# Kernel tuning notes

Measured on AMD Instinct MI355X. Metric: run time of the kernel, lower is better.

The kernel has to match this reference:

```python
import jax, jax.numpy as jnp
import numpy as np

DN = ('NCHW', 'OIHW', 'NCHW')


def conv(x, W, s, p):
    return jax.lax.conv_general_dilated(x, W, (s, s), [(p, p), (p, p)], dimension_numbers=DN)


def conv_t(y, W, s, p, op):
    # F.conv_transpose2d(y, W, stride=s, padding=p, output_padding=op)
    k = W.shape[2]
    Wt = jnp.flip(W, (2, 3)).transpose(1, 0, 2, 3)  # (I,O,k,k) -> OIHW for the transpose conv
    pad = (k - 1 - p, k - 1 - p + op)
    return jax.lax.conv_general_dilated(y, Wt, (1, 1), [pad, pad], lhs_dilation=(s, s), dimension_numbers=DN)


def build_blk(weight_specs, ms, g, n):
    # blk_diag[r, c, g, m, n'] accumulation exactly as in the torch nested loops
    blk = jnp.zeros((ms, ms, g, n, n), dtype=weight_specs[0][0].dtype)
    for (W, stride, k) in weight_specs:
        A = W.reshape(W.shape[0], g, n, k, k)  # (O, g, n, k, k)
        ATA = jnp.einsum('ogmab,ognab->abgmn', A, A)  # (k, k, g, n, n)
        offset = ((stride - k) // 2) % stride  # k odd branch of the torch code
        for i1 in range(k):
            for j1 in range(k):
                for r in range((i1 + offset) % stride, ms, stride):
                    for c in range((j1 + offset) % stride, ms, stride):
                        blk = blk.at[r, c].add(ATA[i1, j1])
    return blk


def sub_diag(Z, X, blk, ms, g, n):
    b, c, h, w = X.shape
    X0 = X.reshape(b, g, n, h // ms, ms, w // ms, ms)
    Yd = jnp.einsum('rcgmn,bgnhrwc->bgmhrwc', blk, X0)
    return Z - Yd.reshape(b, c, h, w)


def hollow_forward(x0, x1, W00, W10, W11, b0, b1, g):
    # multiply: Y_i = sum_j conv(X_j)
    Y0 = conv(x0, W00, 1, 2)                       # (B,16,258,258)
    Y1 = conv(x0, W10, 2, 3) + conv(x1, W11, 1, 2)  # (B,32,130,130)
    # multiply_transpose: Z_j = sum_i conv_t(Y_i)
    Z0 = conv_t(Y0, W00, 1, 2, 0) + conv_t(Y1, W10, 2, 3, 1)  # (B,16,256,256)
    Z1 = conv_t(Y1, W11, 1, 2, 0)                             # (B,32,128,128)
    # block-diagonal self-term subtraction
    blk0 = build_blk([(W00, 1, 3), (W10, 2, 3)], ms=2, g=1, n=16)
    blk1 = build_blk([(W11, 1, 3)], ms=1, g=2, n=16)
    Z0 = sub_diag(Z0, x0, blk0, 2, 1, 16)
    Z1 = sub_diag(Z1, x1, blk1, 1, 2, 16)
    # bias term: y -= bias/||bias|| * g[i]; return -y
    Z0 = Z0 - (b0 / jnp.linalg.norm(b0)) * g[0]
    Z1 = Z1 - (b1 / jnp.linalg.norm(b1)) * g[1]
    return (-Z0, -Z1)


def setup_inputs() -> dict:
    key = jax.random.key(0)
    ks = jax.random.split(key, 8)
    B = 16
    x0 = jax.random.normal(ks[0], (B, 16, 256, 256), dtype=jnp.float32)
    x1 = jax.random.normal(ks[1], (B, 32, 128, 128), dtype=jnp.float32)
    # conv weights (PyTorch OIHW layout), modest scale ~ 1/sqrt(fan_in*k*k)
    W00 = jax.random.normal(ks[2], (16, 16, 3, 3), dtype=jnp.float32) * 0.08
    W10 = jax.random.normal(ks[3], (32, 16, 3, 3), dtype=jnp.float32) * 0.08
    W11 = jax.random.normal(ks[4], (32, 32, 3, 3), dtype=jnp.float32) * 0.06
    b0 = jax.random.uniform(ks[5], (16, 256, 256), dtype=jnp.float32)
    b1 = jax.random.uniform(ks[6], (32, 128, 128), dtype=jnp.float32)
    g = jnp.ones((2,), dtype=jnp.float32)
    return {'x0': x0, 'x1': x1, 'W00': W00, 'W10': W10, 'W11': W11, 'b0': b0, 'b1': b1, 'g': g}


def reference(x0, x1, W00, W10, W11, b0, b1, g):
    return hollow_forward(x0, x1, W00, W10, W11, b0, b1, g)
```

## Files before the change

kernel.cpp:

```cpp
#include <hip/hip_runtime.h>
#include <stdint.h>


using short8 = __attribute__((ext_vector_type(8))) short;
using f32x4  = __attribute__((ext_vector_type(4))) float;

#define B_ 16

static constexpr size_t Y1T_OFF  = 0;
static constexpr size_t Y1T_ROWB = 132 * 64;
static constexpr size_t X1T_OFF  = (size_t)16 * 130 * 132 * 64;
static constexpr size_t AB0_OFF  = X1T_OFF + (size_t)16 * 128 * 128 * 64;
static constexpr size_t AB1_OFF  = AB0_OFF + 24 * 1024;
static constexpr size_t SUM_OFF  = AB1_OFF + 20 * 1024;
static constexpr size_t AB2_OFF  = SUM_OFF + 1024;

__device__ __forceinline__ uint32_t bf16rne(float v) {
  uint32_t u = __float_as_uint(v);
  return (u + 0x7fffu + ((u >> 16) & 1u)) >> 16;
}
__device__ __forceinline__ uint32_t packbf(float lo, float hi) {
  return bf16rne(lo) | (bf16rne(hi) << 16);
}
__device__ __forceinline__ f32x4 mfma16(short8 a, short8 b, f32x4 c) {
  return __builtin_amdgcn_mfma_f32_16x16x32_bf16(a, b, c, 0, 0, 0);
}
__device__ __forceinline__ int xcd_swz(int bid, int chunk) {
  return (bid & 7) * chunk + (bid >> 3);
}

__global__ void blob_k(const float* __restrict__ W00, const float* __restrict__ W10,
                       const float* __restrict__ W11, char* __restrict__ ws) {
  int e = blockIdx.x * 256 + threadIdx.x;
  if (e < 2) ((float*)(ws + SUM_OFF))[e] = 0.f;
  if (e < 12288) {
    int chunk = e >> 9, le = e & 511, lane = le >> 3, j = le & 7;
    int q = lane >> 4, m = lane & 15;
    float val = 0.f;
    if (chunk < 13) {
      int t = 2 * chunk + (q >> 1);
      int n = ((q & 1) << 3) + j;
      if (t <= 24 && t != 12) {
        int dy = t / 5 - 2, dx = t % 5 - 2;
        for (int o = 0; o < 16; ++o) {
          const float* wm = W00 + (o * 16 + m) * 9;
          const float* wn = W00 + (o * 16 + n) * 9;
          for (int ay = 0; ay < 3; ++ay) {
            int ay2 = ay + dy; if ((unsigned)ay2 > 2u) continue;
            for (int ax = 0; ax < 3; ++ax) {
              int ax2 = ax + dx; if ((unsigned)ax2 > 2u) continue;
              val += wm[ay * 3 + ax] * wn[ay2 * 3 + ax2];
            }
          }
        }
      }
    } else if (chunk < 22) {
      int tap = chunk - 13;
      int o = ((lane >> 4) << 3) + j;
      val = W10[(o * 16 + m) * 9 + tap];
    } else {
      int py = chunk - 22;
      int k = ((lane >> 4) << 3) + j;
      int par = k >> 4, n = k & 15;
      for (int o = 0; o < 32; ++o) {
        const float* wn = W10 + (o * 16 + n) * 9;
        const float* wm = W10 + (o * 16 + m) * 9;
        for (int by = 0; by < 3; ++by) {
          if ((py == 0) ? (by != 1) : (by == 1)) continue;
          for (int bx = 0; bx < 3; ++bx) {
            if ((par == 0) ? (bx != 1) : (bx == 1)) continue;
            val -= wn[by * 3 + bx] * wm[by * 3 + bx];
          }
        }
      }
    }
    ((uint16_t*)(ws + AB0_OFF))[chunk * 512 + lane * 8 + j] = (uint16_t)bf16rne(val);
  } else if (e < 12288 + 10240) {
    int e2 = e - 12288;
    int chunk = e2 >> 10, r = e2 & 1023, h = r >> 9, le = r & 511;
    int lane = le >> 3, j = le & 7;
    int m = h * 16 + (lane & 15);
    int kk = ((lane >> 4) << 3) + j;
    float val = 0.f;
    if (chunk < 9) {
      val = W11[(kk * 32 + m) * 9 + chunk];
    } else if ((kk >> 4) == h) {
      int np = kk & 15;
      float s = 0.f;
      for (int o = 0; o < 32; ++o)
        for (int t = 0; t < 9; ++t)
          s += W11[(o * 32 + m) * 9 + t] * W11[(o * 32 + h * 16 + np) * 9 + t];
      val = -s;
    }
    ((uint16_t*)(ws + AB1_OFF))[(chunk * 2 + h) * 512 + lane * 8 + j] = (uint16_t)bf16rne(val);
  } else if (e < 12288 + 10240 + 28672) {
    int e3 = e - 22528;
    int chunk = e3 >> 9, le = e3 & 511;
    int lane = le >> 3, j = le & 7;
    int q = lane >> 4, m = lane & 15;
    int k = q * 8 + j;
    int part;
    float val = 0.f;
    if (chunk < 36) {
      int t = chunk >> 2, h = (chunk >> 1) & 1;
      part = chunk & 1;
      int o = h * 16 + m;
      val = W11[(o * 32 + k) * 9 + t];
    } else {
      int c2 = chunk - 36;
      int c5 = c2 >> 2, h = (c2 >> 1) & 1;
      part = c2 & 1;
      int tap = 2 * c5 + (k >> 4);
      int o = h * 16 + m;
      if (tap <= 8) val = W10[(o * 16 + (k & 15)) * 9 + tap];
    }
    uint32_t hi = bf16rne(val);
    uint16_t outv;
    if (part == 0) outv = (uint16_t)hi;
    else outv = (uint16_t)bf16rne(val - __uint_as_float(hi << 16));
    ((uint16_t*)(ws + AB2_OFF))[chunk * 512 + lane * 8 + j] = outv;
  }
}

__global__ void sumsq_k(const float* __restrict__ src, int n, float* __restrict__ dst) {
  float s = 0.f;
  for (int i = blockIdx.x * blockDim.x + threadIdx.x; i < n; i += gridDim.x * blockDim.x) {
    float v = src[i];
    s += v * v;
  }
  #pragma unroll
  for (int off = 32; off > 0; off >>= 1) s += __shfl_down(s, off, 64);
  if ((threadIdx.x & 63) == 0) atomicAdd(dst, s);
}

__global__ __launch_bounds__(256) void x1t_k(const float* __restrict__ x1, char* __restrict__ ws) {
  __shared__ __align__(16) uint16_t tmp[128 * 32];
  int b = blockIdx.x >> 7, r = blockIdx.x & 127;
  int tid = threadIdx.x;
  for (int e = tid; e < 4096; e += 256) {
    int ch = e >> 7, c = e & 127;
    float v = x1[((size_t)(b * 32 + ch) * 128 + r) * 128 + c];
    tmp[c * 32 + ch] = (uint16_t)bf16rne(v);
  }
  __syncthreads();
  char* dst = ws + X1T_OFF + ((size_t)(b * 128 + r) * 128) * 64;
  for (int e = tid; e < 512; e += 256)
    *(short8*)(dst + e * 16) = *(const short8*)((const char*)tmp + e * 16);
}

__global__ __launch_bounds__(256, 5) void y1m_k(const float* __restrict__ x0,
                                                char* __restrict__ ws) {
  __shared__ __align__(16) uint16_t x0s[2 * 3 * 2 * 146 * 8];
  int tid = threadIdx.x;
  int bid = xcd_swz(blockIdx.x, 260);
  int b = bid / 130, iy = bid % 130;

  {
    uint4 z = make_uint4(0u, 0u, 0u, 0u);
    for (int e = tid; e < 1752; e += 256) ((uint4*)x0s)[e] = z;
  }
  __syncthreads();

  {
    const float* x0b = x0 + (size_t)b * 1048576;
    for (int e = tid; e < 6144; e += 256) {
      int r = e >> 11;
      int ch0 = ((e >> 8) & 7) * 2;
      int c = e & 255;
      int gy = 2 * iy + r - 3;
      float v0 = 0.f, v1 = 0.f;
      if ((unsigned)gy < 256u) {
        const float* rp = x0b + (size_t)ch0 * 65536 + (size_t)gy * 256 + c;
        v0 = rp[0]; v1 = rp[65536];
      }
      int sc = c + 3, p = sc & 1, hc = sc >> 1;
      *(uint32_t*)((char*)x0s + ((((ch0 >> 3) * 3 + r) * 2 + p) * 146 + hc) * 16 + (ch0 & 7) * 2)
          = packbf(v0, v1);
    }
  }

  int lane = tid & 63, wv = tid >> 6;
  int nn = lane & 15, q = lane >> 4, qh = q >> 1, ql = q & 1;
  const char* ab2 = ws + AB2_OFF;
  const char* x1tb = ws + X1T_OFF;

  f32x4 a00 = {0.f,0.f,0.f,0.f}, a01 = {0.f,0.f,0.f,0.f};
  f32x4 a10 = {0.f,0.f,0.f,0.f}, a11 = {0.f,0.f,0.f,0.f};
  f32x4 a20 = {0.f,0.f,0.f,0.f}, a21 = {0.f,0.f,0.f,0.f};
  const short8 z8 = {0,0,0,0,0,0,0,0};

  #pragma unroll
  for (int t = 0; t < 9; ++t) {
    const int ay = t / 3, ax = t % 3;
    const char* cb = ab2 + t * 4096 + lane * 16;
    short8 Ah0 = *(const short8*)(cb);
    short8 Al0 = *(const short8*)(cb + 1024);
    short8 Ah1 = *(const short8*)(cb + 2048);
    short8 Al1 = *(const short8*)(cb + 3072);
    int gy = iy + ay - 2;
    bool rowok = ((unsigned)gy < 128u);
    const char* rb = x1tb + ((size_t)(b * 128 + (rowok ? gy : 0))) * 8192 + q * 16;
    int c0 = (wv << 4) + nn + ax - 2;
    bool ok0 = rowok && ((unsigned)c0 < 128u);
    short8 B0 = *(const short8*)(rb + (size_t)(ok0 ? c0 : 0) * 64);
    if (!ok0) B0 = z8;
    int c1 = c0 + 64;
    bool ok1 = rowok && ((unsigned)c1 < 128u);
    short8 B1 = *(const short8*)(rb + (size_t)(ok1 ? c1 : 0) * 64);
    if (!ok1) B1 = z8;
    a00 = mfma16(Ah0, B0, a00); a00 = mfma16(Al0, B0, a00);
    a01 = mfma16(Ah1, B0, a01); a01 = mfma16(Al1, B0, a01);
    a10 = mfma16(Ah0, B1, a10); a10 = mfma16(Al0, B1, a10);
    a11 = mfma16(Ah1, B1, a11); a11 = mfma16(Al1, B1, a11);
    if (wv == 0) {
      int c2 = c0 + 128;
      bool ok2 = rowok && ((unsigned)c2 < 128u);
      short8 B2 = *(const short8*)(rb + (size_t)(ok2 ? c2 : 0) * 64);
      if (!ok2) B2 = z8;
      a20 = mfma16(Ah0, B2, a20); a20 = mfma16(Al0, B2, a20);
      a21 = mfma16(Ah1, B2, a21); a21 = mfma16(Al1, B2, a21);
    }
  }

  __syncthreads();

  #pragma unroll
  for (int c5 = 0; c5 < 5; ++c5) {
    const char* cb = ab2 + (36 + c5 * 4) * 1024 + lane * 16;
    short8 Ah0 = *(const short8*)(cb);
    short8 Al0 = *(const short8*)(cb + 1024);
    short8 Ah1 = *(const short8*)(cb + 2048);
    short8 Al1 = *(const short8*)(cb + 3072);
    int tl = 2 * c5 + qh; if (tl > 8) tl = 8;
    int by = tl / 3, bx = tl % 3;
    int p = bx & 1, hb = bx >> 1;
    const char* bb = (const char*)x0s + ((((ql * 3 + by) * 2 + p) * 146) + hb + nn) * 16 + wv * 256;
    short8 B0 = *(const short8*)(bb);
    short8 B1 = *(const short8*)(bb + 1024);
    a00 = mfma16(Ah0, B0, a00); a00 = mfma16(Al0, B0, a00);
    a01 = mfma16(Ah1, B0, a01); a01 = mfma16(Al1, B0, a01);
    a10 = mfma16(Ah0, B1, a10); a10 = mfma16(Al0, B1, a10);
    a11 = mfma16(Ah1, B1, a11); a11 = mfma16(Al1, B1, a11);
    if (wv == 0) {
      short8 B2 = *(const short8*)(bb + 2048);
      a20 = mfma16(Ah0, B2, a20); a20 = mfma16(Al0, B2, a20);
      a21 = mfma16(Ah1, B2, a21); a21 = mfma16(Al1, B2, a21);
    }
  }

  char* yp = ws + Y1T_OFF + (size_t)(b * 130 + iy) * Y1T_ROWB;
  auto st = [&](int f, f32x4 v0, f32x4 v1) {
    int ix = f * 16 + nn;
    if (ix < 130) {
      uint64_t lo = (uint64_t)packbf(v0[0], v0[1]) | ((uint64_t)packbf(v0[2], v0[3]) << 32);
      uint64_t hi = (uint64_t)packbf(v1[0], v1[1]) | ((uint64_t)packbf(v1[2], v1[3]) << 32);
      *(uint64_t*)(yp + ix * 64 + q * 8) = lo;
      *(uint64_t*)(yp + ix * 64 + 32 + q * 8) = hi;
    }
  };
  st(wv, a00, a01);
  st(wv + 4, a10, a11);
  if (wv == 0) st(8, a20, a21);
}

__global__ __launch_bounds__(256, 5) void out0_k(const float* __restrict__ x0,
                                                 const float* __restrict__ b0,
                                                 const float* __restrict__ gg,
                                                 const char* __restrict__ ws,
                                                 float* __restrict__ out) {
  __shared__ __align__(16) uint16_t x0s[2 * 5 * 132 * 8];
  __shared__ __align__(16) uint16_t y1s[4 * 2 * 66 * 8];
  int tid = threadIdx.x;
  int bid = xcd_swz(blockIdx.x, 1024);
  int b = bid >> 9, jy = (bid >> 1) & 255;
  int jx_base = (bid & 1) << 7;

  {
    const float* x0b = x0 + (size_t)b * 1048576;
    for (int e = tid; e < 1320; e += 256) {
      int c = e % 132, rr = e / 132, r = rr % 5, oct = rr / 5;
      int gy = jy + r - 2, gx = jx_base + c - 2;
      uint32_t w0 = 0u, w1 = 0u, w2 = 0u, w3 = 0u;
      if ((unsigned)gy < 256u && (unsigned)gx < 256u) {
        const float* p = x0b + (size_t)(oct * 8) * 65536 + gy * 256 + gx;
        w0 = packbf(p[0],      p[65536]);
        w1 = packbf(p[131072], p[196608]);
        w2 = packbf(p[262144], p[327680]);
        w3 = packbf(p[393216], p[458752]);
      }
      *(uint4*)((char*)x0s + (size_t)e * 16) = make_uint4(w0, w1, w2, w3);
    }
  }
  {
    const char* y1tb = ws + Y1T_OFF;
    int uy = jy >> 1, c0 = jx_base >> 1;
    for (int e = tid; e < 528; e += 256) {
      int qq = e & 3, t = e >> 2, lc = t % 66, ry = t / 66;
      short8 v = *(const short8*)(y1tb +
          ((size_t)(b * 130 + uy + 1 + ry) * 132 + c0 + lc) * 64 + qq * 16);
      *(short8*)((char*)y1s + ((size_t)(qq * 2 + ry) * 66 + lc) * 16) = v;
    }
  }
  __syncthreads();

  int lane = tid & 63, wv = tid >> 6;
  int nn = lane & 15, q = lane >> 4, qh = q >> 1, ql = q & 1;
  const char* ab0 = ws + AB0_OFF;
  f32x4 acc[2];
  #pragma unroll
  for (int i = 0; i < 2; ++i) { acc[i][0]=0.f; acc[i][1]=0.f; acc[i][2]=0.f; acc[i][3]=0.f; }

  const uint16_t* xsl = x0s + ql * 5280;
  const uint16_t* ysl = y1s + q * 1056;
  int pxb = wv * 32 + nn;

  #pragma unroll
  for (int c = 0; c < 13; ++c) {
    short8 A = *(const short8*)(ab0 + c * 1024 + lane * 16);
    const int tA = 2 * c;
    const int tB = (2 * c + 1 > 24) ? 24 : 2 * c + 1;
    const int offA = ((tA / 5) * 132 + (tA % 5)) * 8;
    const int offB = ((tB / 5) * 132 + (tB % 5)) * 8;
    int toff = qh ? offB : offA;
    const uint16_t* base = xsl + toff + pxb * 8;
    short8 B0 = *(const short8*)(base);
    short8 B1 = *(const short8*)(base + 128);
    acc[0] = mfma16(A, B0, acc[0]);
    acc[1] = mfma16(A, B1, acc[1]);
  }

  {
    const short8 z8 = {0,0,0,0,0,0,0,0};
    if ((jy & 1) == 0) {
      #pragma unroll
      for (int bx = 0; bx < 3; ++bx) {
        short8 A = *(const short8*)(ab0 + (16 + bx) * 1024 + lane * 16);
        bool keep = (((nn + 3 - bx) & 1) == 0);
        int cb = (nn + 3 - bx) >> 1;
        const uint16_t* base = ysl + (cb + wv * 16) * 8;
        short8 B0 = *(const short8*)(base);
        short8 B1 = *(const short8*)(base + 64);
        if (!keep) { B0 = z8; B1 = z8; }
        acc[0] = mfma16(A, B0, acc[0]);
        acc[1] = mfma16(A, B1, acc[1]);
      }
    } else {
      #pragma unroll
      for (int s = 0; s < 2; ++s) {
        const int chunkb = s ? 19 : 13;
        const int rybase = s ? 0 : 1;
        #pragma unroll
        for (int bx = 0; bx < 3; ++bx) {
          short8 A = *(const short8*)(ab0 + (chunkb + bx) * 1024 + lane * 16);
          bool keep = (((nn + 3 - bx) & 1) == 0);
          int cb = (nn + 3 - bx) >> 1;
          const uint16_t* base = ysl + (rybase * 66 + cb + wv * 16) * 8;
          short8 B0 = *(const short8*)(base);
          short8 B1 = *(const short8*)(base + 64);
          if (!keep) { B0 = z8; B1 = z8; }
          acc[0] = mfma16(A, B0, acc[0]);
          acc[1] = mfma16(A, B1, acc[1]);
        }
      }
    }
  }

  {
    const short8 z8 = {0,0,0,0,0,0,0,0};
    short8 A = *(const short8*)(ab0 + (22 + (jy & 1)) * 1024 + lane * 16);
    const uint16_t* base = xsl + (2 * 132 + 2) * 8 + pxb * 8;
    short8 B0 = *(const short8*)(base);
    short8 B1 = *(const short8*)(base + 128);
    bool keep = ((nn & 1) == qh);
    if (!keep) { B0 = z8; B1 = z8; }
    acc[0] = mfma16(A, B0, acc[0]);
    acc[1] = mfma16(A, B1, acc[1]);
  }

  float rs0 = gg[0] / sqrtf(((const float*)(ws + SUM_OFF))[0]);
  #pragma unroll
  for (int i = 0; i < 2; ++i) {
    int px = jx_base + wv * 32 + i * 16 + nn;
    #pragma unroll
    for (int reg = 0; reg < 4; ++reg) {
      int m = q * 4 + reg;
      size_t boff = ((size_t)m * 256 + jy) * 256 + px;
      out[((size_t)(b * 16 + m) * 256 + jy) * 256 + px] = b0[boff] * rs0 - acc[i][reg];
    }
  }
}

__global__ __launch_bounds__(256) void out1_k(const float* __restrict__ b1,
                                              const float* __restrict__ gg,
                                              const char* __restrict__ ws,
                                              float* __restrict__ out) {
  __shared__ __align__(16) uint16_t ys[4 * 3 * 132 * 8];
  __shared__ __align__(16) uint16_t x1s[4 * 128 * 8];
  int tid = threadIdx.x;
  int bid = xcd_swz(blockIdx.x, 256);
  int b = bid >> 7, jy = bid & 127;
  const char* y1tb = ws + Y1T_OFF;
  const char* x1tb = ws + X1T_OFF;
  for (int e = tid; e < 1584; e += 256) {
    int row = e / 528, rr = e % 528, c = rr >> 2, qq = rr & 3;
    short8 v = *(const short8*)(y1tb + ((size_t)(b * 130 + jy + row) * 132 + c) * 64 + qq * 16);
    *(short8*)(ys + qq * 3168 + (row * 132 + c) * 8) = v;
  }
  for (int e = tid; e < 512; e += 256) {
    int c = e >> 2, qq = e & 3;
    short8 v = *(const short8*)(x1tb + ((size_t)(b * 128 + jy) * 128 + c) * 64 + qq * 16);
    *(short8*)(x1s + qq * 1024 + c * 8) = v;
  }
  __syncthreads();

  int lane = tid & 63, wv = tid >> 6;
  int nn = lane & 15, q = lane >> 4;
  const char* ab1 = ws + AB1_OFF;
  f32x4 acc[2][2];
  #pragma unroll
  for (int i = 0; i < 2; ++i)
    #pragma unroll
    for (int h = 0; h < 2; ++h) { acc[i][h][0]=0.f; acc[i][h][1]=0.f; acc[i][h][2]=0.f; acc[i][h][3]=0.f; }

  const uint16_t* ysl = ys + q * 3168;
  const uint16_t* xsl = x1s + q * 1024;
  int pxb = wv * 32 + nn;

  #pragma unroll
  for (int t = 0; t < 9; ++t) {
    const int ay = t / 3, ax = t % 3;
    short8 A0 = *(const short8*)(ab1 + (t * 2 + 0) * 1024 + lane * 16);
    short8 A1 = *(const short8*)(ab1 + (t * 2 + 1) * 1024 + lane * 16);
    const uint16_t* base = ysl + ((2 - ay) * 132 + (2 - ax) + pxb) * 8;
    short8 B0 = *(const short8*)(base);
    short8 B1 = *(const short8*)(base + 128);
    acc[0][0] = mfma16(A0, B0, acc[0][0]);
    acc[0][1] = mfma16(A1, B0, acc[0][1]);
    acc[1][0] = mfma16(A0, B1, acc[1][0]);
    acc[1][1] = mfma16(A1, B1, acc[1][1]);
  }
  {
    short8 A0 = *(const short8*)(ab1 + 18 * 1024 + lane * 16);
    short8 A1 = *(const short8*)(ab1 + 19 * 1024 + lane * 16);
    const uint16_t* base = xsl + pxb * 8;
    short8 B0 = *(const short8*)(base);
    short8 B1 = *(const short8*)(base + 128);
    acc[0][0] = mfma16(A0, B0, acc[0][0]);
    acc[0][1] = mfma16(A1, B0, acc[0][1]);
    acc[1][0] = mfma16(A0, B1, acc[1][0]);
    acc[1][1] = mfma16(A1, B1, acc[1][1]);
  }

  float rs1 = gg[1] / sqrtf(((const float*)(ws + SUM_OFF))[1]);
  #pragma unroll
  for (int i = 0; i < 2; ++i) {
    int px = wv * 32 + i * 16 + nn;
    #pragma unroll
    for (int h = 0; h < 2; ++h)
      #pragma unroll
      for (int reg = 0; reg < 4; ++reg) {
        int m = h * 16 + q * 4 + reg;
        size_t boff = ((size_t)m * 128 + jy) * 128 + px;
        out[16777216 + ((size_t)(b * 32 + m) * 128 + jy) * 128 + px] = b1[boff] * rs1 - acc[i][h][reg];
      }
  }
}

extern "C" void kernel_launch(void* const* d_in, const int* in_sizes, int n_in,
                              void* d_out, int out_size, void* d_ws, size_t ws_size,
                              hipStream_t stream) {
  const float* x0  = (const float*)d_in[0];
  const float* x1  = (const float*)d_in[1];
  const float* W00 = (const float*)d_in[2];
  const float* W10 = (const float*)d_in[3];
  const float* W11 = (const float*)d_in[4];
  const float* b0  = (const float*)d_in[5];
  const float* b1  = (const float*)d_in[6];
  const float* g   = (const float*)d_in[7];
  float* out = (float*)d_out;
  char* ws   = (char*)d_ws;

  blob_k<<<200, 256, 0, stream>>>(W00, W10, W11, ws);
  sumsq_k<<<512, 256, 0, stream>>>(b0, 16 * 256 * 256, (float*)(ws + SUM_OFF));
  sumsq_k<<<512, 256, 0, stream>>>(b1, 32 * 128 * 128, (float*)(ws + SUM_OFF) + 1);
  x1t_k<<<2048, 256, 0, stream>>>(x1, ws);
  y1m_k<<<16 * 130, 256, 0, stream>>>(x0, ws);
  out0_k<<<8192, 256, 0, stream>>>(x0, b0, g, ws, out);
  out1_k<<<2048, 256, 0, stream>>>(b1, g, ws, out);
}
```

Before: 371.5 us.

## Merge seven launches into three kernels and drop atomic norm reduction

Result: faster. 319.8 us (-13.9%).

```diff
diff --git a/kernel.cpp b/kernel.cpp
--- a/kernel.cpp
+++ b/kernel.cpp
@@ -14,6 +14,7 @@
 static constexpr size_t AB1_OFF  = AB0_OFF + 24 * 1024;
 static constexpr size_t SUM_OFF  = AB1_OFF + 20 * 1024;
 static constexpr size_t AB2_OFF  = SUM_OFF + 1024;
+static constexpr size_t PART_OFF = AB2_OFF + 56 * 1024;
 
 __device__ __forceinline__ uint32_t bf16rne(float v) {
   uint32_t u = __float_as_uint(v);
@@ -29,129 +30,166 @@
   return (bid & 7) * chunk + (bid >> 3);
 }
 
-__global__ void blob_k(const float* __restrict__ W00, const float* __restrict__ W10,
-                       const float* __restrict__ W11, char* __restrict__ ws) {
-  int e = blockIdx.x * 256 + threadIdx.x;
-  if (e < 2) ((float*)(ws + SUM_OFF))[e] = 0.f;
-  if (e < 12288) {
-    int chunk = e >> 9, le = e & 511, lane = le >> 3, j = le & 7;
-    int q = lane >> 4, m = lane & 15;
-    float val = 0.f;
-    if (chunk < 13) {
-      int t = 2 * chunk + (q >> 1);
-      int n = ((q & 1) << 3) + j;
-      if (t <= 24 && t != 12) {
-        int dy = t / 5 - 2, dx = t % 5 - 2;
-        for (int o = 0; o < 16; ++o) {
-          const float* wm = W00 + (o * 16 + m) * 9;
-          const float* wn = W00 + (o * 16 + n) * 9;
-          for (int ay = 0; ay < 3; ++ay) {
-            int ay2 = ay + dy; if ((unsigned)ay2 > 2u) continue;
-            for (int ax = 0; ax < 3; ++ax) {
-              int ax2 = ax + dx; if ((unsigned)ax2 > 2u) continue;
-              val += wm[ay * 3 + ax] * wn[ay2 * 3 + ax2];
+__global__ __launch_bounds__(256) void prep_k(const float* __restrict__ x1,
+                                              const float* __restrict__ W00,
+                                              const float* __restrict__ W10,
+                                              const float* __restrict__ W11,
+                                              const float* __restrict__ b0,
+                                              const float* __restrict__ b1,
+                                              char* __restrict__ ws) {
+  __shared__ __align__(16) uint16_t tmp[128 * 32];
+  int raw = blockIdx.x, tid = threadIdx.x;
+
+  if (raw < 2048) {
+    int b = raw >> 7, r = raw & 127;
+    for (int e = tid; e < 4096; e += 256) {
+      int ch = e >> 7, c = e & 127;
+      float v = x1[((size_t)(b * 32 + ch) * 128 + r) * 128 + c];
+      tmp[c * 32 + ch] = (uint16_t)bf16rne(v);
+    }
+    __syncthreads();
+    char* dst = ws + X1T_OFF + ((size_t)(b * 128 + r) * 128) * 64;
+    for (int e = tid; e < 512; e += 256)
+      *(short8*)(dst + e * 16) = *(const short8*)((const char*)tmp + e * 16);
+    return;
+  }
+
+  if (raw < 2248) {
+    int e = (raw - 2048) * 256 + tid;
+    if (e < 12288) {
+      int chunk = e >> 9, le = e & 511, lane = le >> 3, j = le & 7;
+      int q = lane >> 4, m = lane & 15;
+      float val = 0.f;
+      if (chunk < 13) {
+        int t = 2 * chunk + (q >> 1);
+        int n = ((q & 1) << 3) + j;
+        if (t <= 24 && t != 12) {
+          int dy = t / 5 - 2, dx = t % 5 - 2;
+          for (int o = 0; o < 16; ++o) {
+            const float* wm = W00 + (o * 16 + m) * 9;
+            const float* wn = W00 + (o * 16 + n) * 9;
+            for (int ay = 0; ay < 3; ++ay) {
+              int ay2 = ay + dy; if ((unsigned)ay2 > 2u) continue;
+              for (int ax = 0; ax < 3; ++ax) {
+                int ax2 = ax + dx; if ((unsigned)ax2 > 2u) continue;
+                val += wm[ay * 3 + ax] * wn[ay2 * 3 + ax2];
+              }
             }
           }
         }
-      }
-    } else if (chunk < 22) {
-      int tap = chunk - 13;
-      int o = ((lane >> 4) << 3) + j;
-      val = W10[(o * 16 + m) * 9 + tap];
-    } else {
-      int py = chunk - 22;
-      int k = ((lane >> 4) << 3) + j;
-      int par = k >> 4, n = k & 15;
-      for (int o = 0; o < 32; ++o) {
-        const float* wn = W10 + (o * 16 + n) * 9;
-        const float* wm = W10 + (o * 16 + m) * 9;
-        for (int by = 0; by < 3; ++by) {
-          if ((py == 0) ? (by != 1) : (by == 1)) continue;
-          for (int bx = 0; bx < 3; ++bx) {
-            if ((par == 0) ? (bx != 1) : (bx == 1)) continue;
-            val -= wn[by * 3 + bx] * wm[by * 3 + bx];
+      } else if (chunk < 22) {
+        int tap = chunk - 13;
+        int o = ((lane >> 4) << 3) + j;
+        val = W10[(o * 16 + m) * 9 + tap];
+      } else {
+        int py = chunk - 22;
+        int k = ((lane >> 4) << 3) + j;
+        int par = k >> 4, n = k & 15;
+        for (int o = 0; o < 32; ++o) {
+          const float* wn = W10 + (o * 16 + n) * 9;
+          const float* wm = W10 + (o * 16 + m) * 9;
+          for (int by = 0; by < 3; ++by) {
+            if ((py == 0) ? (by != 1) : (by == 1)) continue;
+            for (int bx = 0; bx < 3; ++bx) {
+              if ((par == 0) ? (bx != 1) : (bx == 1)) continue;
+              val -= wn[by * 3 + bx] * wm[by * 3 + bx];
+            }
           }
         }
       }
-    }
-    ((uint16_t*)(ws + AB0_OFF))[chunk * 512 + lane * 8 + j] = (uint16_t)bf16rne(val);
-  } else if (e < 12288 + 10240) {
-    int e2 = e - 12288;
-    int chunk = e2 >> 10, r = e2 & 1023, h = r >> 9, le = r & 511;
-    int lane = le >> 3, j = le & 7;
-    int m = h * 16 + (lane & 15);
-    int kk = ((lane >> 4) << 3) + j;
-    float val = 0.f;
-    if (chunk < 9) {
-      val = W11[(kk * 32 + m) * 9 + chunk];
-    } else if ((kk >> 4) == h) {
-      int np = kk & 15;
-      float s = 0.f;
-      for (int o = 0; o < 32; ++o)
-        for (int t = 0; t < 9; ++t)
-          s += W11[(o * 32 + m) * 9 + t] * W11[(o * 32 + h * 16 + np) * 9 + t];
-      val = -s;
-    }
-    ((uint16_t*)(ws + AB1_OFF))[(chunk * 2 + h) * 512 + lane * 8 + j] = (uint16_t)bf16rne(val);
-  } else if (e < 12288 + 10240 + 28672) {
-    int e3 = e - 22528;
-    int chunk = e3 >> 9, le = e3 & 511;
-    int lane = le >> 3, j = le & 7;
-    int q = lane >> 4, m = lane & 15;
-    int k = q * 8 + j;
-    int part;
-    float val = 0.f;
-    if (chunk < 36) {
-      int t = chunk >> 2, h = (chunk >> 1) & 1;
-      part = chunk & 1;
-      int o = h * 16 + m;
-      val = W11[(o * 32 + k) * 9 + t];
-    } else {
-      int c2 = chunk - 36;
-      int c5 = c2 >> 2, h = (c2 >> 1) & 1;
-      part = c2 & 1;
-      int tap = 2 * c5 + (k >> 4);
-      int o = h * 16 + m;
-      if (tap <= 8) val = W10[(o * 16 + (k & 15)) * 9 + tap];
-    }
-    uint32_t hi = bf16rne(val);
-    uint16_t outv;
-    if (part == 0) outv = (uint16_t)hi;
-    else outv = (uint16_t)bf16rne(val - __uint_as_float(hi << 16));
-    ((uint16_t*)(ws + AB2_OFF))[chunk * 512 + lane * 8 + j] = outv;
-  }
-}
-
-__global__ void sumsq_k(const float* __restrict__ src, int n, float* __restrict__ dst) {
-  float s = 0.f;
-  for (int i = blockIdx.x * blockDim.x + threadIdx.x; i < n; i += gridDim.x * blockDim.x) {
-    float v = src[i];
-    s += v * v;
-  }
-  #pragma unroll
-  for (int off = 32; off > 0; off >>= 1) s += __shfl_down(s, off, 64);
-  if ((threadIdx.x & 63) == 0) atomicAdd(dst, s);
-}
-
-__global__ __launch_bounds__(256) void x1t_k(const float* __restrict__ x1, char* __restrict__ ws) {
-  __shared__ __align__(16) uint16_t tmp[128 * 32];
-  int b = blockIdx.x >> 7, r = blockIdx.x & 127;
-  int tid = threadIdx.x;
-  for (int e = tid; e < 4096; e += 256) {
-    int ch = e >> 7, c = e & 127;
-    float v = x1[((size_t)(b * 32 + ch) * 128 + r) * 128 + c];
-    tmp[c * 32 + ch] = (uint16_t)bf16rne(v);
-  }
-  __syncthreads();
-  char* dst = ws + X1T_OFF + ((size_t)(b * 128 + r) * 128) * 64;
-  for (int e = tid; e < 512; e += 256)
-    *(short8*)(dst + e * 16) = *(const short8*)((const char*)tmp + e * 16);
+      ((uint16_t*)(ws + AB0_OFF))[chunk * 512 + lane * 8 + j] = (uint16_t)bf16rne(val);
+    } else if (e < 12288 + 10240) {
+      int e2 = e - 12288;
+      int chunk = e2 >> 10, r = e2 & 1023, h = r >> 9, le = r & 511;
+      int lane = le >> 3, j = le & 7;
+      int m = h * 16 + (lane & 15);
+      int kk = ((lane >> 4) << 3) + j;
+      float val = 0.f;
+      if (chunk < 9) {
+        val = W11[(kk * 32 + m) * 9 + chunk];
+      } else if ((kk >> 4) == h) {
+        int np = kk & 15;
+        float s = 0.f;
+        for (int o = 0; o < 32; ++o)
+          for (int t = 0; t < 9; ++t)
+            s += W11[(o * 32 + m) * 9 + t] * W11[(o * 32 + h * 16 + np) * 9 + t];
+        val = -s;
+      }
+      ((uint16_t*)(ws + AB1_OFF))[(chunk * 2 + h) * 512 + lane * 8 + j] = (uint16_t)bf16rne(val);
+    } else if (e < 12288 + 10240 + 28672) {
+      int e3 = e - 22528;
+      int chunk = e3 >> 9, le = e3 & 511;
+      int lane = le >> 3, j = le & 7;
+      int q = lane >> 4, m = lane & 15;
+      int k = q * 8 + j;
+      int part;
+      float val = 0.f;
+      if (chunk < 36) {
+        int t = chunk >> 2, h = (chunk >> 1) & 1;
+        part = chunk & 1;
+        int o = h * 16 + m;
+        val = W11[(o * 32 + k) * 9 + t];
+      } else {
+        int c2 = chunk - 36;
+        int c5 = c2 >> 2, h = (c2 >> 1) & 1;
+        part = c2 & 1;
+        int tap = 2 * c5 + (k >> 4);
+        int o = h * 16 + m;
+        if (tap <= 8) val = W10[(o * 16 + (k & 15)) * 9 + tap];
+      }
+      uint32_t hi = bf16rne(val);
+      uint16_t outv;
+      if (part == 0) outv = (uint16_t)hi;
+      else outv = (uint16_t)bf16rne(val - __uint_as_float(hi << 16));
+      ((uint16_t*)(ws + AB2_OFF))[chunk * 512 + lane * 8 + j] = outv;
+    }
+    return;
+  }
+
+  float* part = (float*)(ws + PART_OFF);
+  if (raw < 2312) {
+    int blk = raw - 2248;
+    float s = 0.f;
+    for (int i = blk * 256 + tid; i < 1048576; i += 64 * 256) {
+      float v = b0[i]; s += v * v;
+    }
+    #pragma unroll
+    for (int off = 32; off > 0; off >>= 1) s += __shfl_down(s, off, 64);
+    if ((tid & 63) == 0) part[blk * 4 + (tid >> 6)] = s;
+  } else {
+    int blk = raw - 2312;
+    float s = 0.f;
+    for (int i = blk * 256 + tid; i < 524288; i += 32 * 256) {
+      float v = b1[i]; s += v * v;
+    }
+    #pragma unroll
+    for (int off = 32; off > 0; off >>= 1) s += __shfl_down(s, off, 64);
+    if ((tid & 63) == 0) part[256 + blk * 4 + (tid >> 6)] = s;
+  }
 }
 
 __global__ __launch_bounds__(256, 5) void y1m_k(const float* __restrict__ x0,
                                                 char* __restrict__ ws) {
   __shared__ __align__(16) uint16_t x0s[2 * 3 * 2 * 146 * 8];
   int tid = threadIdx.x;
+  if (blockIdx.x >= 2080) {
+    if (blockIdx.x == 2080) {
+      int lane = tid & 63, wvv = tid >> 6;
+      const float* part = (const float*)(ws + PART_OFF);
+      if (wvv == 0) {
+        float s = part[lane * 4] + part[lane * 4 + 1] + part[lane * 4 + 2] + part[lane * 4 + 3];
+        #pragma unroll
+        for (int off = 32; off > 0; off >>= 1) s += __shfl_down(s, off, 64);
+        if (lane == 0) ((float*)(ws + SUM_OFF))[0] = s;
+      } else if (wvv == 1) {
+        float s = part[256 + lane * 2] + part[256 + lane * 2 + 1];
+        #pragma unroll
+        for (int off = 32; off > 0; off >>= 1) s += __shfl_down(s, off, 64);
+        if (lane == 0) ((float*)(ws + SUM_OFF))[1] = s;
+      }
+    }
+    return;
+  }
   int bid = xcd_swz(blockIdx.x, 260);
   int b = bid / 130, iy = bid % 130;
 
@@ -263,206 +301,191 @@
   if (wv == 0) st(8, a20, a21);
 }
 
-__global__ __launch_bounds__(256, 5) void out0_k(const float* __restrict__ x0,
+__global__ __launch_bounds__(256, 5) void outs_k(const float* __restrict__ x0,
                                                  const float* __restrict__ b0,
+                                                 const float* __restrict__ b1,
                                                  const float* __restrict__ gg,
                                                  const char* __restrict__ ws,
                                                  float* __restrict__ out) {
-  __shared__ __align__(16) uint16_t x0s[2 * 5 * 132 * 8];
-  __shared__ __align__(16) uint16_t y1s[4 * 2 * 66 * 8];
-  int tid = threadIdx.x;
-  int bid = xcd_swz(blockIdx.x, 1024);
-  int b = bid >> 9, jy = (bid >> 1) & 255;
-  int jx_base = (bid & 1) << 7;
-
-  {
-    const float* x0b = x0 + (size_t)b * 1048576;
-    for (int e = tid; e < 1320; e += 256) {
-      int c = e % 132, rr = e / 132, r = rr % 5, oct = rr / 5;
-      int gy = jy + r - 2, gx = jx_base + c - 2;
-      uint32_t w0 = 0u, w1 = 0u, w2 = 0u, w3 = 0u;
-      if ((unsigned)gy < 256u && (unsigned)gx < 256u) {
-        const float* p = x0b + (size_t)(oct * 8) * 65536 + gy * 256 + gx;
-        w0 = packbf(p[0],      p[65536]);
-        w1 = packbf(p[131072], p[196608]);
-        w2 = packbf(p[262144], p[327680]);
-        w3 = packbf(p[393216], p[458752]);
-      }
-      *(uint4*)((char*)x0s + (size_t)e * 16) = make_uint4(w0, w1, w2, w3);
-    }
-  }
-  {
-    const char* y1tb = ws + Y1T_OFF;
-    int uy = jy >> 1, c0 = jx_base >> 1;
-    for (int e = tid; e < 528; e += 256) {
-      int qq = e & 3, t = e >> 2, lc = t % 66, ry = t / 66;
-      short8 v = *(const short8*)(y1tb +
-          ((size_t)(b * 130 + uy + 1 + ry) * 132 + c0 + lc) * 64 + qq * 16);
-      *(short8*)((char*)y1s + ((size_t)(qq * 2 + ry) * 66 + lc) * 16) = v;
-    }
-  }
-  __syncthreads();
-
+  __shared__ __align__(16) uint16_t smem[2 * 5 * 132 * 8 + 4 * 2 * 66 * 8];
+  int raw = blockIdx.x, tid = threadIdx.x;
   int lane = tid & 63, wv = tid >> 6;
-  int nn = lane & 15, q = lane >> 4, qh = q >> 1, ql = q & 1;
-  const char* ab0 = ws + AB0_OFF;
-  f32x4 acc[2];
-  #pragma unroll
-  for (int i = 0; i < 2; ++i) { acc[i][0]=0.f; acc[i][1]=0.f; acc[i][2]=0.f; acc[i][3]=0.f; }
-
-  const uint16_t* xsl = x0s + ql * 5280;
-  const uint16_t* ysl = y1s + q * 1056;
-  int pxb = wv * 32 + nn;
-
-  #pragma unroll
-  for (int c = 0; c < 13; ++c) {
-    short8 A = *(const short8*)(ab0 + c * 1024 + lane * 16);
-    const int tA = 2 * c;
-    const int tB = (2 * c + 1 > 24) ? 24 : 2 * c + 1;
-    const int offA = ((tA / 5) * 132 + (tA % 5)) * 8;
-    const int offB = ((tB / 5) * 132 + (tB % 5)) * 8;
-    int toff = qh ? offB : offA;
-    const uint16_t* base = xsl + toff + pxb * 8;
-    short8 B0 = *(const short8*)(base);
-    short8 B1 = *(const short8*)(base + 128);
-    acc[0] = mfma16(A, B0, acc[0]);
-    acc[1] = mfma16(A, B1, acc[1]);
-  }
-
-  {
-    const short8 z8 = {0,0,0,0,0,0,0,0};
-    if ((jy & 1) == 0) {
-      #pragma unroll
-      for (int bx = 0; bx < 3; ++bx) {
-        short8 A = *(const short8*)(ab0 + (16 + bx) * 1024 + lane * 16);
-        bool keep = (((nn + 3 - bx) & 1) == 0);
-        int cb = (nn + 3 - bx) >> 1;
-        const uint16_t* base = ysl + (cb + wv * 16) * 8;
-        short8 B0 = *(const short8*)(base);
-        short8 B1 = *(const short8*)(base + 64);
-        if (!keep) { B0 = z8; B1 = z8; }
-        acc[0] = mfma16(A, B0, acc[0]);
-        acc[1] = mfma16(A, B1, acc[1]);
-      }
-    } else {
-      #pragma unroll
-      for (int s = 0; s < 2; ++s) {
-        const int chunkb = s ? 19 : 13;
-        const int rybase = s ? 0 : 1;
+  int nn = lane & 15, q = lane >> 4;
+
+  if (raw < 8192) {
+    uint16_t* x0s = smem;
+    uint16_t* y1s = smem + 2 * 5 * 132 * 8;
+    int bid = xcd_swz(raw, 1024);
+    int b = bid >> 9, jy = (bid >> 1) & 255;
+    int jx_base = (bid & 1) << 7;
+
+    {
+      const float* x0b = x0 + (size_t)b * 1048576;
+      for (int e = tid; e < 1320; e += 256) {
+        int c = e % 132, rr = e / 132, r = rr % 5, oct = rr / 5;
+        int gy = jy + r - 2, gx = jx_base + c - 2;
+        uint32_t w0 = 0u, w1 = 0u, w2 = 0u, w3 = 0u;
+        if ((unsigned)gy < 256u && (unsigned)gx < 256u) {
+          const float* p = x0b + (size_t)(oct * 8) * 65536 + gy * 256 + gx;
+          w0 = packbf(p[0],      p[65536]);
+          w1 = packbf(p[131072], p[196608]);
+          w2 = packbf(p[262144], p[327680]);
+          w3 = packbf(p[393216], p[458752]);
+        }
+        *(uint4*)((char*)x0s + (size_t)e * 16) = make_uint4(w0, w1, w2, w3);
+      }
+    }
+    {
+      const char* y1tb = ws + Y1T_OFF;
+      int uy = jy >> 1, c0 = jx_base >> 1;
+      for (int e = tid; e < 528; e += 256) {
+        int qq = e & 3, t = e >> 2, lc = t % 66, ry = t / 66;
+        short8 v = *(const short8*)(y1tb +
+            ((size_t)(b * 130 + uy + 1 + ry) * 132 + c0 + lc) * 64 + qq * 16);
+        *(short8*)((char*)y1s + ((size_t)(qq * 2 + ry) * 66 + lc) * 16) = v;
+      }
+    }
+    __syncthreads();
+
+    int qh = q >> 1, ql = q & 1;
+    const char* ab0 = ws + AB0_OFF;
+    f32x4 acc[2];
+    #pragma unroll
+    for (int i = 0; i < 2; ++i) { acc[i][0]=0.f; acc[i][1]=0.f; acc[i][2]=0.f; acc[i][3]=0.f; }
+
+    const uint16_t* xsl = x0s + ql * 5280;
+    const uint16_t* ysl = y1s + q * 1056;
+    int pxb = wv * 32 + nn;
+
+    #pragma unroll
+    for (int c = 0; c < 13; ++c) {
+      short8 A = *(const short8*)(ab0 + c * 1024 + lane * 16);
+      const int tA = 2 * c;
+      const int tB = (2 * c + 1 > 24) ? 24 : 2 * c + 1;
+      const int offA = ((tA / 5) * 132 + (tA % 5)) * 8;
+      const int offB = ((tB / 5) * 132 + (tB % 5)) * 8;
+      int toff = qh ? offB : offA;
+      const uint16_t* base = xsl + toff + pxb * 8;
+      short8 B0 = *(const short8*)(base);
+      short8 B1 = *(const short8*)(base + 128);
+      acc[0] = mfma16(A, B0, acc[0]);
+      acc[1] = mfma16(A, B1, acc[1]);
+    }
+
+    {
+      const short8 z8 = {0,0,0,0,0,0,0,0};
+      if ((jy & 1) == 0) {
         #pragma unroll
         for (int bx = 0; bx < 3; ++bx) {
-          short8 A = *(const short8*)(ab0 + (chunkb + bx) * 1024 + lane * 16);
+          short8 A = *(const short8*)(ab0 + (16 + bx) * 1024 + lane * 16);
           bool keep = (((nn + 3 - bx) & 1) == 0);
           int cb = (nn + 3 - bx) >> 1;
-          const uint16_t* base = ysl + (rybase * 66 + cb + wv * 16) * 8;
+          const uint16_t* base = ysl + (cb + wv * 16) * 8;
           short8 B0 = *(const short8*)(base);
           short8 B1 = *(const short8*)(base + 64);
           if (!keep) { B0 = z8; B1 = z8; }
           acc[0] = mfma16(A, B0, acc[0]);
           acc[1] = mfma16(A, B1, acc[1]);
         }
-      }
-    }
-  }
-
-  {
-    const short8 z8 = {0,0,0,0,0,0,0,0};
-    short8 A = *(const short8*)(ab0 + (22 + (jy & 1)) * 1024 + lane * 16);
-    const uint16_t* base = xsl + (2 * 132 + 2) * 8 + pxb * 8;
-    short8 B0 = *(const short8*)(base);
-    short8 B1 = *(const short8*)(base + 128);
-    bool keep = ((nn & 1) == qh);
-    if (!keep) { B0 = z8; B1 = z8; }
-    acc[0] = mfma16(A, B0, acc[0]);
-    acc[1] = mfma16(A, B1, acc[1]);
-  }
-
-  float rs0 = gg[0] / sqrtf(((const float*)(ws + SUM_OFF))[0]);
-  #pragma unroll
-  for (int i = 0; i < 2; ++i) {
-    int px = jx_base + wv * 32 + i * 16 + nn;
-    #pragma unroll
-    for (int reg = 0; reg < 4; ++reg) {
-      int m = q * 4 + reg;
-      size_t boff = ((size_t)m * 256 + jy) * 256 + px;
-      out[((size_t)(b * 16 + m) * 256 + jy) * 256 + px] = b0[boff] * rs0 - acc[i][reg];
-    }
-  }
-}
-
-__global__ __launch_bounds__(256) void out1_k(const float* __restrict__ b1,
-                                              const float* __restrict__ gg,
-                                              const char* __restrict__ ws,
-                                              float* __restrict__ out) {
-  __shared__ __align__(16) uint16_t ys[4 * 3 * 132 * 8];
-  __shared__ __align__(16) uint16_t x1s[4 * 128 * 8];
-  int tid = threadIdx.x;
-  int bid = xcd_swz(blockIdx.x, 256);
-  int b = bid >> 7, jy = bid & 127;
-  const char* y1tb = ws + Y1T_OFF;
-  const char* x1tb = ws + X1T_OFF;
-  for (int e = tid; e < 1584; e += 256) {
-    int row = e / 528, rr = e % 528, c = rr >> 2, qq = rr & 3;
-    short8 v = *(const short8*)(y1tb + ((size_t)(b * 130 + jy + row) * 132 + c) * 64 + qq * 16);
-    *(short8*)(ys + qq * 3168 + (row * 132 + c) * 8) = v;
-  }
-  for (int e = tid; e < 512; e += 256) {
-    int c = e >> 2, qq = e & 3;
-    short8 v = *(const short8*)(x1tb + ((size_t)(b * 128 + jy) * 128 + c) * 64 + qq * 16);
-    *(short8*)(x1s + qq * 1024 + c * 8) = v;
-  }
-  __syncthreads();
-
-  int lane = tid & 63, wv = tid >> 6;
-  int nn = lane & 15, q = lane >> 4;
-  const char* ab1 = ws + AB1_OFF;
-  f32x4 acc[2][2];
-  #pragma unroll
-  for (int i = 0; i < 2; ++i)
-    #pragma unroll
-    for (int h = 0; h < 2; ++h) { acc[i][h][0]=0.f; acc[i][h][1]=0.f; acc[i][h][2]=0.f; acc[i][h][3]=0.f; }
-
-  const uint16_t* ysl = ys + q * 3168;
-  const uint16_t* xsl = x1s + q * 1024;
-  int pxb = wv * 32 + nn;
-
-  #pragma unroll
-  for (int t = 0; t < 9; ++t) {
-    const int ay = t / 3, ax = t % 3;
-    short8 A0 = *(const short8*)(ab1 + (t * 2 + 0) * 1024 + lane * 16);
-    short8 A1 = *(const short8*)(ab1 + (t * 2 + 1) * 1024 + lane * 16);
-    const uint16_t* base = ysl + ((2 - ay) * 132 + (2 - ax) + pxb) * 8;
-    short8 B0 = *(const short8*)(base);
-    short8 B1 = *(const short8*)(base + 128);
-    acc[0][0] = mfma16(A0, B0, acc[0][0]);
-    acc[0][1] = mfma16(A1, B0, acc[0][1]);
-    acc[1][0] = mfma16(A0, B1, acc[1][0]);
-    acc[1][1] = mfma16(A1, B1, acc[1][1]);
-  }
-  {
-    short8 A0 = *(const short8*)(ab1 + 18 * 1024 + lane * 16);
-    short8 A1 = *(const short8*)(ab1 + 19 * 1024 + lane * 16);
-    const uint16_t* base = xsl + pxb * 8;
-    short8 B0 = *(const short8*)(base);
-    short8 B1 = *(const short8*)(base + 128);
-    acc[0][0] = mfma16(A0, B0, acc[0][0]);
-    acc[0][1] = mfma16(A1, B0, acc[0][1]);
-    acc[1][0] = mfma16(A0, B1, acc[1][0]);
-    acc[1][1] = mfma16(A1, B1, acc[1][1]);
-  }
-
-  float rs1 = gg[1] / sqrtf(((const float*)(ws + SUM_OFF))[1]);
-  #pragma unroll
-  for (int i = 0; i < 2; ++i) {
-    int px = wv * 32 + i * 16 + nn;
-    #pragma unroll
-    for (int h = 0; h < 2; ++h)
+      } else {
+        #pragma unroll
+        for (int s = 0; s < 2; ++s) {
+          const int chunkb = s ? 19 : 13;
+          const int rybase = s ? 0 : 1;
+          #pragma unroll
+          for (int bx = 0; bx < 3; ++bx) {
+            short8 A = *(const short8*)(ab0 + (chunkb + bx) * 1024 + lane * 16);
+            bool keep = (((nn + 3 - bx) & 1) == 0);
+            int cb = (nn + 3 - bx) >> 1;
+            const uint16_t* base = ysl + (rybase * 66 + cb + wv * 16) * 8;
+            short8 B0 = *(const short8*)(base);
+            short8 B1 = *(const short8*)(base + 64);
+            if (!keep) { B0 = z8; B1 = z8; }
+            acc[0] = mfma16(A, B0, acc[0]);
+            acc[1] = mfma16(A, B1, acc[1]);
+          }
+        }
+      }
+    }
+
+    {
+      const short8 z8 = {0,0,0,0,0,0,0,0};
+      short8 A = *(const short8*)(ab0 + (22 + (jy & 1)) * 1024 + lane * 16);
+      const uint16_t* base = xsl + (2 * 132 + 2) * 8 + pxb * 8;
+      short8 B0 = *(const short8*)(base);
+      short8 B1 = *(const short8*)(base + 128);
+      bool keep = ((nn & 1) == qh);
+      if (!keep) { B0 = z8; B1 = z8; }
+      acc[0] = mfma16(A, B0, acc[0]);
+      acc[1] = mfma16(A, B1, acc[1]);
+    }
+
+    float rs0 = gg[0] / sqrtf(((const float*)(ws + SUM_OFF))[0]);
+    #pragma unroll
+    for (int i = 0; i < 2; ++i) {
+      int px = jx_base + wv * 32 + i * 16 + nn;
       #pragma unroll
       for (int reg = 0; reg < 4; ++reg) {
-        int m = h * 16 + q * 4 + reg;
-        size_t boff = ((size_t)m * 128 + jy) * 128 + px;
-        out[16777216 + ((size_t)(b * 32 + m) * 128 + jy) * 128 + px] = b1[boff] * rs1 - acc[i][h][reg];
-      }
+        int m = q * 4 + reg;
+        size_t boff = ((size_t)m * 256 + jy) * 256 + px;
+        out[((size_t)(b * 16 + m) * 256 + jy) * 256 + px] = b0[boff] * rs0 - acc[i][reg];
+      }
+    }
+    return;
+  }
+
+  {
+    int bid = xcd_swz(raw - 8192, 256);
+    int b = bid >> 7, jy = bid & 127;
+    const char* ab1 = ws + AB1_OFF;
+    const char* yb = ws + Y1T_OFF + ((size_t)(b * 130 + jy) * 132) * 64 + q * 16;
+    const char* xb = ws + X1T_OFF + ((size_t)(b * 128 + jy) * 128) * 64 + q * 16;
+    f32x4 acc[2][2];
+    #pragma unroll
+    for (int i = 0; i < 2; ++i)
+      #pragma unroll
+      for (int h = 0; h < 2; ++h) { acc[i][h][0]=0.f; acc[i][h][1]=0.f; acc[i][h][2]=0.f; acc[i][h][3]=0.f; }
+
+    int pxb = wv * 32 + nn;
+
+    #pragma unroll
+    for (int t = 0; t < 9; ++t) {
+      const int ay = t / 3, ax = t % 3;
+      short8 A0 = *(const short8*)(ab1 + (t * 2 + 0) * 1024 + lane * 16);
+      short8 A1 = *(const short8*)(ab1 + (t * 2 + 1) * 1024 + lane * 16);
+      const char* base = yb + (size_t)((2 - ay) * 132 + (2 - ax) + pxb) * 64;
+      short8 B0 = *(const short8*)(base);
+      short8 B1 = *(const short8*)(base + 1024);
+      acc[0][0] = mfma16(A0, B0, acc[0][0]);
+      acc[0][1] = mfma16(A1, B0, acc[0][1]);
+      acc[1][0] = mfma16(A0, B1, acc[1][0]);
+      acc[1][1] = mfma16(A1, B1, acc[1][1]);
+    }
+    {
+      short8 A0 = *(const short8*)(ab1 + 18 * 1024 + lane * 16);
+      short8 A1 = *(const short8*)(ab1 + 19 * 1024 + lane * 16);
+      const char* base = xb + (size_t)pxb * 64;
+      short8 B0 = *(const short8*)(base);
+      short8 B1 = *(const short8*)(base + 1024);
+      acc[0][0] = mfma16(A0, B0, acc[0][0]);
+      acc[0][1] = mfma16(A1, B0, acc[0][1]);
+      acc[1][0] = mfma16(A0, B1, acc[1][0]);
+      acc[1][1] = mfma16(A1, B1, acc[1][1]);
+    }
+
+    float rs1 = gg[1] / sqrtf(((const float*)(ws + SUM_OFF))[1]);
+    #pragma unroll
+    for (int i = 0; i < 2; ++i) {
+      int px = wv * 32 + i * 16 + nn;
+      #pragma unroll
+      for (int h = 0; h < 2; ++h)
+        #pragma unroll
+        for (int reg = 0; reg < 4; ++reg) {
+          int m = h * 16 + q * 4 + reg;
+          size_t boff = ((size_t)m * 128 + jy) * 128 + px;
+          out[16777216 + ((size_t)(b * 32 + m) * 128 + jy) * 128 + px] = b1[boff] * rs1 - acc[i][h][reg];
+        }
+    }
   }
 }
 
@@ -480,11 +503,7 @@
   float* out = (float*)d_out;
   char* ws   = (char*)d_ws;
 
-  blob_k<<<200, 256, 0, stream>>>(W00, W10, W11, ws);
-  sumsq_k<<<512, 256, 0, stream>>>(b0, 16 * 256 * 256, (float*)(ws + SUM_OFF));
-  sumsq_k<<<512, 256, 0, stream>>>(b1, 32 * 128 * 128, (float*)(ws + SUM_OFF) + 1);
-  x1t_k<<<2048, 256, 0, stream>>>(x1, ws);
-  y1m_k<<<16 * 130, 256, 0, stream>>>(x0, ws);
-  out0_k<<<8192, 256, 0, stream>>>(x0, b0, g, ws, out);
-  out1_k<<<2048, 256, 0, stream>>>(b1, g, ws, out);
-}
+  prep_k<<<2344, 256, 0, stream>>>(x1, W00, W10, W11, b0, b1, ws);
+  y1m_k<<<2088, 256, 0, stream>>>(x0, ws);
+  outs_k<<<10240, 256, 0, stream>>>(x0, b0, b1, g, ws, out);
+}
```
